# Performance work log

Measured on AMD Instinct MI355X. Metric: run time of the kernel, lower is better.

The kernel has to match this reference:

```python
import jax, jax.numpy as jnp
import numpy as np

B, S, D, H = 2, 2048, 128, 8  # batch, seq, num_hidden(=head dim), num_heads
EPS = 1e-5


def setup_inputs() -> dict:
    key = jax.random.key(0)
    ks = jax.random.split(key, 12)
    sc = 0.02
    return {
        "query": jax.random.normal(ks[0], (B, S, D), dtype=jnp.float32),
        "Wq": jax.random.normal(ks[1], (2 * H * D, D), dtype=jnp.float32) * sc,
        "bq": jnp.zeros((2 * H * D,), dtype=jnp.float32),
        "Wk": jax.random.normal(ks[2], (2 * H * D, D), dtype=jnp.float32) * sc,
        "bk": jnp.zeros((2 * H * D,), dtype=jnp.float32),
        "Wv": jax.random.normal(ks[3], (H * D, D), dtype=jnp.float32) * sc,
        "bv": jnp.zeros((H * D,), dtype=jnp.float32),
        "Wo": jax.random.normal(ks[4], (D, H * D), dtype=jnp.float32) * sc,
        "bo": jnp.zeros((D,), dtype=jnp.float32),
        "gn_w": jnp.ones((H,), dtype=jnp.float32),
        "gn_b": jnp.zeros((H,), dtype=jnp.float32),
        "lam": jax.random.uniform(ks[5], (), dtype=jnp.float32),
    }


def reference(query, Wq, bq, Wk, bk, Wv, bv, Wo, bo, gn_w, gn_b, lam):
    # Faithful to the torch module: the .view calls are raw reshapes (no
    # transpose), d_k=1 so scale is 1, mask=None path (no causal mask),
    # dropout in eval mode, _lambda == _lambda_init == lam.
    q = (query @ Wq.T + bq).reshape(B, H, S, 2 * D)
    k = (query @ Wk.T + bk).reshape(B, H, S, 2 * D)
    v = (query @ Wv.T + bv).reshape(B, H, S, D)
    q1, q2 = q[..., :D], q[..., D:]
    k1, k2 = k[..., :D], k[..., D:]
    s1 = jnp.einsum("bhqd,bhkd->bhqk", q1, k1)  # / sqrt(d_k=1)
    s2 = jnp.einsum("bhqd,bhkd->bhqk", q2, k2)
    attn = jax.nn.softmax(s1, axis=-1) - lam * jax.nn.softmax(s2, axis=-1)
    out = jnp.einsum("bhqk,bhkd->bhqd", attn, v)          # (B,H,S,D)
    out = out.transpose(0, 2, 1, 3).reshape(B, H, S, D)   # faithful raw reshape
    # GroupNorm(num_groups=H, num_channels=H): normalize per (b, h) over (S, D)
    mean = out.mean(axis=(2, 3), keepdims=True)
    var = out.var(axis=(2, 3), keepdims=True)
    out = (out - mean) * jax.lax.rsqrt(var + EPS)
    out = out * gn_w[None, :, None, None] + gn_b[None, :, None, None]
    out = out * (1.0 - lam)
    # torch.cat([out[:, i] for i in range(H)], dim=-1) -> (B, S, H*D)
    out = out.transpose(0, 2, 1, 3).reshape(B, S, H * D)
    return out @ Wo.T + bo
```

## Files before the change

kernel.cpp:

```cpp
#include <hip/hip_runtime.h>

typedef __bf16 bf16x8 __attribute__((ext_vector_type(8)));
typedef __bf16 bf16x4 __attribute__((ext_vector_type(4)));
typedef float  f32x4  __attribute__((ext_vector_type(4)));

#define MFMA16(a,b,c) __builtin_amdgcn_mfma_f32_16x16x32_bf16((a),(b),(c),0,0,0)

__device__ __forceinline__ bf16x8 cvt8(float4 a, float4 b) {
  bf16x8 v;
  v[0]=(__bf16)a.x; v[1]=(__bf16)a.y; v[2]=(__bf16)a.z; v[3]=(__bf16)a.w;
  v[4]=(__bf16)b.x; v[5]=(__bf16)b.y; v[6]=(__bf16)b.z; v[7]=(__bf16)b.w;
  return v;
}
__device__ __forceinline__ bf16x4 cvt4(float4 a) {
  bf16x4 v;
  v[0]=(__bf16)a.x; v[1]=(__bf16)a.y; v[2]=(__bf16)a.z; v[3]=(__bf16)a.w;
  return v;
}

__global__ void init_out(float* __restrict__ out, const float* __restrict__ bo,
                         float* __restrict__ stats) {
  const int i4 = (blockIdx.x * 256 + threadIdx.x) * 4;
  const float4 b = *(const float4*)(bo + (i4 & 127));
  *(float4*)(out + i4) = b;
  if (blockIdx.x == 0 && threadIdx.x < 32) stats[threadIdx.x] = 0.f;
}

#define LDA 136
__global__ __launch_bounds__(256, 2) void qkv_gemm(
    const float* __restrict__ query,
    const float* __restrict__ Wq, const float* __restrict__ bq,
    const float* __restrict__ Wk, const float* __restrict__ bk,
    const float* __restrict__ Wv, const float* __restrict__ bv,
    __bf16* __restrict__ Qbf, __bf16* __restrict__ Kbf, __bf16* __restrict__ Vbf)
{
  __shared__ __bf16 As[128 * LDA];
  __shared__ __bf16 Bs[128 * LDA];
  const int t = threadIdx.x;
  const int tm = blockIdx.x / 10, ng = blockIdx.x % 10;
  const int m0 = tm * 128;

  const float* abase = query + (long)m0 * 128;
  for (int r = 0; r < 4; ++r) {
    int e = (r*256 + t) * 16;
    int row = e >> 7, col = e & 127;
    const float* sa = abase + row*128 + col;
    *(bf16x8*)&As[row*LDA+col]   = cvt8(*(const float4*)(sa),   *(const float4*)(sa+4));
    *(bf16x8*)&As[row*LDA+col+8] = cvt8(*(const float4*)(sa+8), *(const float4*)(sa+12));
  }

  const int w = t >> 6, lane = t & 63;
  const int lo = lane & 15, quad = lane >> 4;
  const int wm = w >> 1, wn = w & 1;

  for (int nsub = 0; nsub < 4; ++nsub) {
    const int n0 = ng*512 + nsub*128;
    const float* wbase; const float* bias;
    __bf16* obase; int ocol0; int ostride; float oscale;
    if (n0 < 2048)      { wbase = Wq + n0*128;        bias = bq + n0;        obase = Qbf; ocol0 = n0;      ostride = 2048; oscale = 1.4426950408889634f; }
    else if (n0 < 4096) { wbase = Wk + (n0-2048)*128; bias = bk + (n0-2048); obase = Kbf; ocol0 = n0-2048; ostride = 2048; oscale = 1.0f; }
    else                { wbase = Wv + (n0-4096)*128; bias = bv + (n0-4096); obase = Vbf; ocol0 = n0-4096; ostride = 1024; oscale = 1.0f; }

    __syncthreads();
    for (int r = 0; r < 4; ++r) {
      int e = (r*256 + t) * 16;
      int row = e >> 7, col = e & 127;
      const float* sb = wbase + row*128 + col;
      *(bf16x8*)&Bs[row*LDA+col]   = cvt8(*(const float4*)(sb),   *(const float4*)(sb+4));
      *(bf16x8*)&Bs[row*LDA+col+8] = cvt8(*(const float4*)(sb+8), *(const float4*)(sb+12));
    }
    __syncthreads();

    f32x4 acc[4][4];
    #pragma unroll
    for (int i = 0; i < 4; ++i)
      #pragma unroll
      for (int j = 0; j < 4; ++j) acc[i][j] = (f32x4){0.f,0.f,0.f,0.f};

    #pragma unroll
    for (int ks = 0; ks < 4; ++ks) {
      bf16x8 af[4], bfr[4];
      #pragma unroll
      for (int i = 0; i < 4; ++i)
        af[i] = *(const bf16x8*)&As[(wm*64 + i*16 + lo)*LDA + ks*32 + quad*8];
      #pragma unroll
      for (int j = 0; j < 4; ++j)
        bfr[j] = *(const bf16x8*)&Bs[(wn*64 + j*16 + lo)*LDA + ks*32 + quad*8];
      #pragma unroll
      for (int i = 0; i < 4; ++i)
        #pragma unroll
        for (int j = 0; j < 4; ++j)
          acc[i][j] = MFMA16(bfr[j], af[i], acc[i][j]);
    }
    #pragma unroll
    for (int j = 0; j < 4; ++j) {
      const int colb = ocol0 + wn*64 + j*16 + quad*4;
      const f32x4 b4 = *(const f32x4*)(bias + wn*64 + j*16 + quad*4);
      #pragma unroll
      for (int i = 0; i < 4; ++i) {
        const int row = m0 + wm*64 + i*16 + lo;
        bf16x4 v;
        #pragma unroll
        for (int r = 0; r < 4; ++r) v[r] = (__bf16)((acc[i][j][r] + b4[r]) * oscale);
        *(bf16x4*)&obase[(long)row*ostride + colb] = v;
      }
    }
  }
}

__global__ void v_transpose(const __bf16* __restrict__ Vbf, __bf16* __restrict__ Vt)
{
  __shared__ __bf16 tile[128 * 136];
  const int t = threadIdx.x;
  const int bh = blockIdx.x >> 4, st = blockIdx.x & 15;
  const __bf16* src = Vbf + (long)bh*262144 + st*16384;
  for (int r = 0; r < 8; ++r) {
    int e = (r*256 + t) * 8;
    int row = e >> 7, col = e & 127;
    *(bf16x8*)&tile[row*136 + col] = *(const bf16x8*)(src + row*128 + col);
  }
  __syncthreads();
  __bf16* dst = Vt + (long)bh*262144 + st*128;
  for (int r = 0; r < 8; ++r) {
    int e = (r*256 + t) * 8;
    int d = e >> 7, s2c = e & 127;
    bf16x8 v;
    #pragma unroll
    for (int i = 0; i < 8; ++i) v[i] = tile[(s2c + i)*136 + d];
    *(bf16x8*)(dst + d*2048 + s2c) = v;
  }
}

#define LDK 264
#define LDV 40
__global__ __launch_bounds__(256, 2) void attn(
    const __bf16* __restrict__ Qbf, const __bf16* __restrict__ Kbf,
    const __bf16* __restrict__ Vt, float* __restrict__ O,
    const float* __restrict__ lam_p, float* __restrict__ stats)
{
  __shared__ __bf16 Ks[32 * LDK];
  __shared__ __bf16 Vs[128 * LDV];
  __shared__ float red[8];
  const int t = threadIdx.x;
  const int w = t >> 6, lane = t & 63;
  const int lo = lane & 15, quad = lane >> 4;
  const int bh = blockIdx.x & 15, qb = blockIdx.x >> 4;
  const float lam = *lam_p;

  const __bf16* Qh = Qbf + (long)bh*524288;
  const __bf16* Kh = Kbf + (long)bh*524288;
  const __bf16* Vh = Vt  + (long)bh*262144;
  const int qrow0 = qb*64 + w*16;

  bf16x8 qf[8];
  #pragma unroll
  for (int ks = 0; ks < 8; ++ks)
    qf[ks] = *(const bf16x8*)(Qh + (long)(qrow0 + lo)*256 + ks*32 + quad*8);

  f32x4 acc[2][8];
  #pragma unroll
  for (int s = 0; s < 2; ++s)
    #pragma unroll
    for (int mt = 0; mt < 8; ++mt) acc[s][mt] = (f32x4){0.f,0.f,0.f,0.f};
  float lsum[2] = {0.f, 0.f};

  for (int kt = 0; kt < 64; ++kt) {
    __syncthreads();
    {
      const __bf16* ksrc = Kh + (long)kt*8192;
      #pragma unroll
      for (int r = 0; r < 2; ++r) {
        int e = (r*256 + t) * 16;
        int row = e >> 8, col = e & 255;
        int srow = (row & 3) + ((row >> 2) & 1)*16 + ((row >> 3) & 3)*4;
        *(bf16x8*)&Ks[srow*LDK + col]     = *(const bf16x8*)(ksrc + e);
        *(bf16x8*)&Ks[srow*LDK + col + 8] = *(const bf16x8*)(ksrc + e + 8);
      }
    }
    {
      #pragma unroll
      for (int r = 0; r < 2; ++r) {
        int c = r*256 + t;
        int dd = c >> 2, ch = c & 3;
        *(bf16x8*)&Vs[dd*LDV + ch*8] = *(const bf16x8*)(Vh + (long)dd*2048 + kt*32 + ch*8);
      }
    }
    __syncthreads();

    f32x4 s1[2], s2[2];
    #pragma unroll
    for (int nt = 0; nt < 2; ++nt) { s1[nt] = (f32x4){0.f,0.f,0.f,0.f}; s2[nt] = (f32x4){0.f,0.f,0.f,0.f}; }
    #pragma unroll
    for (int nt = 0; nt < 2; ++nt) {
      const int krow = lo + nt*16;
      #pragma unroll
      for (int ks = 0; ks < 4; ++ks) {
        bf16x8 kf = *(const bf16x8*)&Ks[krow*LDK + ks*32 + quad*8];
        s1[nt] = MFMA16(kf, qf[ks], s1[nt]);
      }
      #pragma unroll
      for (int ks = 4; ks < 8; ++ks) {
        bf16x8 kf = *(const bf16x8*)&Ks[krow*LDK + ks*32 + quad*8];
        s2[nt] = MFMA16(kf, qf[ks], s2[nt]);
      }
    }

    bf16x8 pf1, pf2;
    #pragma unroll
    for (int nt = 0; nt < 2; ++nt) {
      #pragma unroll
      for (int r = 0; r < 4; ++r) {
        float p0 = __builtin_exp2f(s1[nt][r]);
        float p1 = __builtin_exp2f(s2[nt][r]);
        lsum[0] += p0;
        lsum[1] += p1;
        pf1[nt*4+r] = (__bf16)p0;
        pf2[nt*4+r] = (__bf16)p1;
      }
    }

    #pragma unroll
    for (int mt = 0; mt < 8; ++mt) {
      bf16x8 vf = *(const bf16x8*)&Vs[(mt*16 + lo)*LDV + quad*8];
      acc[0][mt] = MFMA16(vf, pf1, acc[0][mt]);
      acc[1][mt] = MFMA16(vf, pf2, acc[1][mt]);
    }
  }

  #pragma unroll
  for (int s = 0; s < 2; ++s) {
    lsum[s] += __shfl_xor(lsum[s], 16);
    lsum[s] += __shfl_xor(lsum[s], 32);
  }
  const float inv1 = 1.f / lsum[0];
  const float inv2 = lam / lsum[1];

  float ssum = 0.f, ssq = 0.f;
  float* Oh = O + (long)bh*262144;
  #pragma unroll
  for (int mt = 0; mt < 8; ++mt) {
    f32x4 o;
    #pragma unroll
    for (int r = 0; r < 4; ++r) {
      o[r] = acc[0][mt][r]*inv1 - acc[1][mt][r]*inv2;
      ssum += o[r]; ssq += o[r]*o[r];
    }
    *(f32x4*)(Oh + (long)(qrow0 + lo)*128 + mt*16 + quad*4) = o;
  }
  #pragma unroll
  for (int msk = 1; msk < 64; msk <<= 1) { ssum += __shfl_xor(ssum, msk); ssq += __shfl_xor(ssq, msk); }
  if (lane == 0) { red[w] = ssum; red[4 + w] = ssq; }
  __syncthreads();
  if (t == 0) {
    const int g = (bh >> 3)*8 + (qb >> 2);
    atomicAdd(&stats[g*2],   red[0] + red[1] + red[2] + red[3]);
    atomicAdd(&stats[g*2+1], red[4] + red[5] + red[6] + red[7]);
  }
}

#define LDC 72
__global__ __launch_bounds__(256, 2) void out_gemm(
    const float* __restrict__ O, const float* __restrict__ stats,
    const float* __restrict__ gn_w, const float* __restrict__ gn_b,
    const float* __restrict__ lam_p,
    const float* __restrict__ Wo, float* __restrict__ out)
{
  __shared__ __bf16 As[64 * LDC];
  __shared__ __bf16 Bs[128 * LDC];
  const int t = threadIdx.x;
  const int w = t >> 6, lane = t & 63;
  const int lo = lane & 15, quad = lane >> 4;
  const int m0 = (blockIdx.x & 63) * 64;
  const int kq = blockIdx.x >> 6;
  const int b = m0 >> 11;
  const float lam1 = 1.f - *lam_p;

  const int hp = kq;
  const float sN   = stats[(b*8 + hp)*2];
  const float ssN  = stats[(b*8 + hp)*2 + 1];
  const float mean = sN * (1.f/262144.f);
  const float rstd = rsqrtf(ssN * (1.f/262144.f) - mean*mean + 1e-5f);
  const float gwv  = gn_w[hp] * rstd * lam1;
  const float shv  = (gn_b[hp] - mean * rstd * gn_w[hp]) * lam1;

  f32x4 acc[8];
  #pragma unroll
  for (int j = 0; j < 8; ++j) acc[j] = (f32x4){0.f,0.f,0.f,0.f};

  for (int kc = 0; kc < 2; ++kc) {
    const int k0 = kq*128 + kc*64;
    const int d0 = kc*64;
    __syncthreads();
    for (int r = 0; r < 4; ++r) {
      int e = r*1024 + t*4;
      int row_l = e >> 6, col_l = e & 63;
      const int spp = (m0 + row_l) & 2047;
      const int h = spp & 7, srow = hp*256 + (spp >> 3);
      float4 v = *(const float4*)(O + ((long)(b*8 + h)*2048 + srow)*128 + d0 + col_l);
      float4 o;
      o.x = v.x*gwv + shv; o.y = v.y*gwv + shv; o.z = v.z*gwv + shv; o.w = v.w*gwv + shv;
      *(bf16x4*)&As[row_l*LDC + col_l] = cvt4(o);
    }
    for (int r = 0; r < 8; ++r) {
      int e = (r*256 + t) * 4;
      int row = e >> 6, col = e & 63;
      *(bf16x4*)&Bs[row*LDC + col] = cvt4(*(const float4*)(Wo + (long)row*1024 + k0 + col));
    }
    __syncthreads();
    #pragma unroll
    for (int ks = 0; ks < 2; ++ks) {
      bf16x8 af = *(const bf16x8*)&As[(w*16 + lo)*LDC + ks*32 + quad*8];
      #pragma unroll
      for (int j = 0; j < 8; ++j) {
        bf16x8 bfr = *(const bf16x8*)&Bs[(j*16 + lo)*LDC + ks*32 + quad*8];
        acc[j] = MFMA16(af, bfr, acc[j]);
      }
    }
  }
  #pragma unroll
  for (int j = 0; j < 8; ++j) {
    const int col = j*16 + lo;
    #pragma unroll
    for (int r = 0; r < 4; ++r)
      atomicAdd(&out[(long)(m0 + w*16 + quad*4 + r)*128 + col], acc[j][r]);
  }
}

extern "C" void kernel_launch(void* const* d_in, const int* in_sizes, int n_in,
                              void* d_out, int out_size, void* d_ws, size_t ws_size,
                              hipStream_t stream) {
  const float* query = (const float*)d_in[0];
  const float* Wq = (const float*)d_in[1];
  const float* bq = (const float*)d_in[2];
  const float* Wk = (const float*)d_in[3];
  const float* bk = (const float*)d_in[4];
  const float* Wv = (const float*)d_in[5];
  const float* bv = (const float*)d_in[6];
  const float* Wo = (const float*)d_in[7];
  const float* bo = (const float*)d_in[8];
  const float* gn_w = (const float*)d_in[9];
  const float* gn_b = (const float*)d_in[10];
  const float* lam = (const float*)d_in[11];

  char* ws = (char*)d_ws;
  __bf16* Qbf  = (__bf16*)(ws);
  __bf16* Kbf  = (__bf16*)(ws + 16777216);
  __bf16* Vbf  = (__bf16*)(ws + 33554432);
  __bf16* Vt   = (__bf16*)(ws + 41943040);
  float*  O    = (float* )(ws + 50331648);
  float*  stats= (float* )(ws + 67108864);
  float* out = (float*)d_out;

  init_out   <<<dim3(512),  dim3(256), 0, stream>>>(out, bo, stats);
  qkv_gemm   <<<dim3(320),  dim3(256), 0, stream>>>(query, Wq, bq, Wk, bk, Wv, bv, Qbf, Kbf, Vbf);
  v_transpose<<<dim3(256),  dim3(256), 0, stream>>>(Vbf, Vt);
  attn       <<<dim3(512),  dim3(256), 0, stream>>>(Qbf, Kbf, Vt, O, lam, stats);
  out_gemm   <<<dim3(512),  dim3(256), 0, stream>>>(O, stats, gn_w, gn_b, lam, Wo, out);
}
```

Before: 232.1 us.

## Double-buffer K/V tiles in attention and split QKV GEMM into more blocks

After: 219.2 us. 5.6% less time.

```diff
diff --git a/kernel.cpp b/kernel.cpp
--- a/kernel.cpp
+++ b/kernel.cpp
@@ -37,8 +37,15 @@
   __shared__ __bf16 As[128 * LDA];
   __shared__ __bf16 Bs[128 * LDA];
   const int t = threadIdx.x;
-  const int tm = blockIdx.x / 10, ng = blockIdx.x % 10;
-  const int m0 = tm * 128;
+  const int tile = blockIdx.x;
+  const int tm = tile / 40, tn = tile % 40;
+  const int m0 = tm * 128, n0 = tn * 128;
+
+  const float* wbase; const float* bias;
+  __bf16* obase; int ocol0; int ostride; float oscale;
+  if (n0 < 2048)      { wbase = Wq + n0*128;        bias = bq + n0;        obase = Qbf; ocol0 = n0;      ostride = 2048; oscale = 1.4426950408889634f; }
+  else if (n0 < 4096) { wbase = Wk + (n0-2048)*128; bias = bk + (n0-2048); obase = Kbf; ocol0 = n0-2048; ostride = 2048; oscale = 1.0f; }
+  else                { wbase = Wv + (n0-4096)*128; bias = bv + (n0-4096); obase = Vbf; ocol0 = n0-4096; ostride = 1024; oscale = 1.0f; }
 
   const float* abase = query + (long)m0 * 128;
   for (int r = 0; r < 4; ++r) {
@@ -47,63 +54,48 @@
     const float* sa = abase + row*128 + col;
     *(bf16x8*)&As[row*LDA+col]   = cvt8(*(const float4*)(sa),   *(const float4*)(sa+4));
     *(bf16x8*)&As[row*LDA+col+8] = cvt8(*(const float4*)(sa+8), *(const float4*)(sa+12));
-  }
+    const float* sb = wbase + row*128 + col;
+    *(bf16x8*)&Bs[row*LDA+col]   = cvt8(*(const float4*)(sb),   *(const float4*)(sb+4));
+    *(bf16x8*)&Bs[row*LDA+col+8] = cvt8(*(const float4*)(sb+8), *(const float4*)(sb+12));
+  }
+  __syncthreads();
 
   const int w = t >> 6, lane = t & 63;
   const int lo = lane & 15, quad = lane >> 4;
   const int wm = w >> 1, wn = w & 1;
 
-  for (int nsub = 0; nsub < 4; ++nsub) {
-    const int n0 = ng*512 + nsub*128;
-    const float* wbase; const float* bias;
-    __bf16* obase; int ocol0; int ostride; float oscale;
-    if (n0 < 2048)      { wbase = Wq + n0*128;        bias = bq + n0;        obase = Qbf; ocol0 = n0;      ostride = 2048; oscale = 1.4426950408889634f; }
-    else if (n0 < 4096) { wbase = Wk + (n0-2048)*128; bias = bk + (n0-2048); obase = Kbf; ocol0 = n0-2048; ostride = 2048; oscale = 1.0f; }
-    else                { wbase = Wv + (n0-4096)*128; bias = bv + (n0-4096); obase = Vbf; ocol0 = n0-4096; ostride = 1024; oscale = 1.0f; }
-
-    __syncthreads();
-    for (int r = 0; r < 4; ++r) {
-      int e = (r*256 + t) * 16;
-      int row = e >> 7, col = e & 127;
-      const float* sb = wbase + row*128 + col;
-      *(bf16x8*)&Bs[row*LDA+col]   = cvt8(*(const float4*)(sb),   *(const float4*)(sb+4));
-      *(bf16x8*)&Bs[row*LDA+col+8] = cvt8(*(const float4*)(sb+8), *(const float4*)(sb+12));
-    }
-    __syncthreads();
-
-    f32x4 acc[4][4];
+  f32x4 acc[4][4];
+  #pragma unroll
+  for (int i = 0; i < 4; ++i)
+    #pragma unroll
+    for (int j = 0; j < 4; ++j) acc[i][j] = (f32x4){0.f,0.f,0.f,0.f};
+
+  #pragma unroll
+  for (int ks = 0; ks < 4; ++ks) {
+    bf16x8 af[4], bfr[4];
     #pragma unroll
     for (int i = 0; i < 4; ++i)
-      #pragma unroll
-      for (int j = 0; j < 4; ++j) acc[i][j] = (f32x4){0.f,0.f,0.f,0.f};
-
-    #pragma unroll
-    for (int ks = 0; ks < 4; ++ks) {
-      bf16x8 af[4], bfr[4];
-      #pragma unroll
-      for (int i = 0; i < 4; ++i)
-        af[i] = *(const bf16x8*)&As[(wm*64 + i*16 + lo)*LDA + ks*32 + quad*8];
+      af[i] = *(const bf16x8*)&As[(wm*64 + i*16 + lo)*LDA + ks*32 + quad*8];
+    #pragma unroll
+    for (int j = 0; j < 4; ++j)
+      bfr[j] = *(const bf16x8*)&Bs[(wn*64 + j*16 + lo)*LDA + ks*32 + quad*8];
+    #pragma unroll
+    for (int i = 0; i < 4; ++i)
       #pragma unroll
       for (int j = 0; j < 4; ++j)
-        bfr[j] = *(const bf16x8*)&Bs[(wn*64 + j*16 + lo)*LDA + ks*32 + quad*8];
-      #pragma unroll
-      for (int i = 0; i < 4; ++i)
-        #pragma unroll
-        for (int j = 0; j < 4; ++j)
-          acc[i][j] = MFMA16(bfr[j], af[i], acc[i][j]);
-    }
-    #pragma unroll
-    for (int j = 0; j < 4; ++j) {
-      const int colb = ocol0 + wn*64 + j*16 + quad*4;
-      const f32x4 b4 = *(const f32x4*)(bias + wn*64 + j*16 + quad*4);
-      #pragma unroll
-      for (int i = 0; i < 4; ++i) {
-        const int row = m0 + wm*64 + i*16 + lo;
-        bf16x4 v;
-        #pragma unroll
-        for (int r = 0; r < 4; ++r) v[r] = (__bf16)((acc[i][j][r] + b4[r]) * oscale);
-        *(bf16x4*)&obase[(long)row*ostride + colb] = v;
-      }
+        acc[i][j] = MFMA16(bfr[j], af[i], acc[i][j]);
+  }
+  #pragma unroll
+  for (int j = 0; j < 4; ++j) {
+    const int colb = ocol0 + wn*64 + j*16 + quad*4;
+    const f32x4 b4 = *(const f32x4*)(bias + wn*64 + j*16 + quad*4);
+    #pragma unroll
+    for (int i = 0; i < 4; ++i) {
+      const int row = m0 + wm*64 + i*16 + lo;
+      bf16x4 v;
+      #pragma unroll
+      for (int r = 0; r < 4; ++r) v[r] = (__bf16)((acc[i][j][r] + b4[r]) * oscale);
+      *(bf16x4*)&obase[(long)row*ostride + colb] = v;
     }
   }
 }
@@ -138,8 +130,8 @@
     const __bf16* __restrict__ Vt, float* __restrict__ O,
     const float* __restrict__ lam_p, float* __restrict__ stats)
 {
-  __shared__ __bf16 Ks[32 * LDK];
-  __shared__ __bf16 Vs[128 * LDV];
+  __shared__ __bf16 Ks[2][32 * LDK];
+  __shared__ __bf16 Vs[2][128 * LDV];
   __shared__ float red[8];
   const int t = threadIdx.x;
   const int w = t >> 6, lane = t & 63;
@@ -157,6 +149,31 @@
   for (int ks = 0; ks < 8; ++ks)
     qf[ks] = *(const bf16x8*)(Qh + (long)(qrow0 + lo)*256 + ks*32 + quad*8);
 
+  int ke[2], ksrow[2], kcol[2], vdd[2], vch[2];
+  #pragma unroll
+  for (int r = 0; r < 2; ++r) {
+    ke[r] = (r*256 + t) * 16;
+    const int row = ke[r] >> 8;
+    kcol[r] = ke[r] & 255;
+    ksrow[r] = (row & 3) + ((row >> 2) & 1)*16 + ((row >> 3) & 3)*4;
+    const int c = r*256 + t;
+    vdd[r] = c >> 2; vch[r] = c & 3;
+  }
+
+  bf16x8 kra[2][2], vra[2];
+  #pragma unroll
+  for (int r = 0; r < 2; ++r) {
+    kra[r][0] = *(const bf16x8*)(Kh + ke[r]);
+    kra[r][1] = *(const bf16x8*)(Kh + ke[r] + 8);
+    vra[r]    = *(const bf16x8*)(Vh + (long)vdd[r]*2048 + vch[r]*8);
+  }
+  #pragma unroll
+  for (int r = 0; r < 2; ++r) {
+    *(bf16x8*)&Ks[0][ksrow[r]*LDK + kcol[r]]     = kra[r][0];
+    *(bf16x8*)&Ks[0][ksrow[r]*LDK + kcol[r] + 8] = kra[r][1];
+    *(bf16x8*)&Vs[0][vdd[r]*LDV + vch[r]*8]      = vra[r];
+  }
+
   f32x4 acc[2][8];
   #pragma unroll
   for (int s = 0; s < 2; ++s)
@@ -166,26 +183,16 @@
 
   for (int kt = 0; kt < 64; ++kt) {
     __syncthreads();
-    {
-      const __bf16* ksrc = Kh + (long)kt*8192;
+    if (kt + 1 < 64) {
       #pragma unroll
       for (int r = 0; r < 2; ++r) {
-        int e = (r*256 + t) * 16;
-        int row = e >> 8, col = e & 255;
-        int srow = (row & 3) + ((row >> 2) & 1)*16 + ((row >> 3) & 3)*4;
-        *(bf16x8*)&Ks[srow*LDK + col]     = *(const bf16x8*)(ksrc + e);
-        *(bf16x8*)&Ks[srow*LDK + col + 8] = *(const bf16x8*)(ksrc + e + 8);
-      }
-    }
-    {
-      #pragma unroll
-      for (int r = 0; r < 2; ++r) {
-        int c = r*256 + t;
-        int dd = c >> 2, ch = c & 3;
-        *(bf16x8*)&Vs[dd*LDV + ch*8] = *(const bf16x8*)(Vh + (long)dd*2048 + kt*32 + ch*8);
-      }
-    }
-    __syncthreads();
+        kra[r][0] = *(const bf16x8*)(Kh + (long)(kt+1)*8192 + ke[r]);
+        kra[r][1] = *(const bf16x8*)(Kh + (long)(kt+1)*8192 + ke[r] + 8);
+        vra[r]    = *(const bf16x8*)(Vh + (long)vdd[r]*2048 + (kt+1)*32 + vch[r]*8);
+      }
+    }
+    const __bf16* kb = Ks[kt & 1];
+    const __bf16* vb = Vs[kt & 1];
 
     f32x4 s1[2], s2[2];
     #pragma unroll
@@ -195,12 +202,12 @@
       const int krow = lo + nt*16;
       #pragma unroll
       for (int ks = 0; ks < 4; ++ks) {
-        bf16x8 kf = *(const bf16x8*)&Ks[krow*LDK + ks*32 + quad*8];
+        bf16x8 kf = *(const bf16x8*)&kb[krow*LDK + ks*32 + quad*8];
         s1[nt] = MFMA16(kf, qf[ks], s1[nt]);
       }
       #pragma unroll
       for (int ks = 4; ks < 8; ++ks) {
-        bf16x8 kf = *(const bf16x8*)&Ks[krow*LDK + ks*32 + quad*8];
+        bf16x8 kf = *(const bf16x8*)&kb[krow*LDK + ks*32 + quad*8];
         s2[nt] = MFMA16(kf, qf[ks], s2[nt]);
       }
     }
@@ -221,9 +228,20 @@
 
     #pragma unroll
     for (int mt = 0; mt < 8; ++mt) {
-      bf16x8 vf = *(const bf16x8*)&Vs[(mt*16 + lo)*LDV + quad*8];
+      bf16x8 vf = *(const bf16x8*)&vb[(mt*16 + lo)*LDV + quad*8];
       acc[0][mt] = MFMA16(vf, pf1, acc[0][mt]);
       acc[1][mt] = MFMA16(vf, pf2, acc[1][mt]);
+    }
+
+    if (kt + 1 < 64) {
+      __bf16* kn = Ks[(kt+1) & 1];
+      __bf16* vn = Vs[(kt+1) & 1];
+      #pragma unroll
+      for (int r = 0; r < 2; ++r) {
+        *(bf16x8*)&kn[ksrow[r]*LDK + kcol[r]]     = kra[r][0];
+        *(bf16x8*)&kn[ksrow[r]*LDK + kcol[r] + 8] = kra[r][1];
+        *(bf16x8*)&vn[vdd[r]*LDV + vch[r]*8]      = vra[r];
+      }
     }
   }
 
@@ -352,7 +370,7 @@
   float* out = (float*)d_out;
 
   init_out   <<<dim3(512),  dim3(256), 0, stream>>>(out, bo, stats);
-  qkv_gemm   <<<dim3(320),  dim3(256), 0, stream>>>(query, Wq, bq, Wk, bk, Wv, bv, Qbf, Kbf, Vbf);
+  qkv_gemm   <<<dim3(1280), dim3(256), 0, stream>>>(query, Wq, bq, Wk, bk, Wv, bv, Qbf, Kbf, Vbf);
   v_transpose<<<dim3(256),  dim3(256), 0, stream>>>(Vbf, Vt);
   attn       <<<dim3(512),  dim3(256), 0, stream>>>(Qbf, Kbf, Vt, O, lam, stats);
   out_gemm   <<<dim3(512),  dim3(256), 0, stream>>>(O, stats, gn_w, gn_b, lam, Wo, out);
```
